# Performance work log

Hardware: AMD Instinct MI355X
Metric: run time of the kernel (lower is better)

Reference implementation:

```python
import jax, jax.numpy as jnp
import numpy as np

D_INPUT, D_MODEL, D_STATE, D_DISCR, KER = 1024, 2048, 16, 128, 4

def setup_inputs() -> dict:
    key = jax.random.key(0)
    ks = jax.random.split(key, 10)
    sc = lambda fan_in: 1.0 / np.sqrt(fan_in)
    seq = jax.random.normal(ks[0], (2, 1024, D_INPUT), dtype=jnp.float32)
    W_in = jax.random.uniform(ks[1], (2 * D_MODEL, D_INPUT), jnp.float32, -sc(D_INPUT), sc(D_INPUT))
    W_out = jax.random.uniform(ks[2], (D_INPUT, D_MODEL), jnp.float32, -sc(D_MODEL), sc(D_MODEL))
    W_sB = jax.random.uniform(ks[3], (D_STATE, D_MODEL), jnp.float32, -sc(D_MODEL), sc(D_MODEL))
    W_sC = jax.random.uniform(ks[4], (D_STATE, D_MODEL), jnp.float32, -sc(D_MODEL), sc(D_MODEL))
    W_sD1 = jax.random.uniform(ks[5], (D_DISCR, D_MODEL), jnp.float32, -sc(D_MODEL), sc(D_MODEL))
    W_sD2 = jax.random.uniform(ks[6], (D_MODEL, D_DISCR), jnp.float32, -sc(D_DISCR), sc(D_DISCR))
    conv_w = jax.random.uniform(ks[7], (D_MODEL, 1, KER), jnp.float32, -sc(KER), sc(KER))
    conv_b = jax.random.uniform(ks[8], (D_MODEL,), jnp.float32, -sc(KER), sc(KER))
    A_param = jnp.tile(jnp.arange(1, D_STATE + 1, dtype=jnp.float32), (D_MODEL, 1))
    D_param = jnp.ones((D_MODEL,), dtype=jnp.float32)
    return dict(seq=seq, W_in=W_in, W_out=W_out, W_sB=W_sB, W_sC=W_sC,
                W_sD1=W_sD1, W_sD2=W_sD2, conv_w=conv_w, conv_b=conv_b,
                A_param=A_param, D_param=D_param)

def _mamba_fwd(seq, W_in, W_out, W_sB, W_sC, W_sD1, W_sD2, conv_w, conv_b, A_param, D_param):
    b, l, _ = seq.shape
    ab = seq @ W_in.T                                   # [b,l,2*dm]
    a, g = jnp.split(ab, 2, axis=-1)
    # causal depthwise conv: torch pads ker-1 both sides then trims [..., :l]
    x = jnp.swapaxes(a, 1, 2)                           # [b,dm,l]
    y = jax.lax.conv_general_dilated(
        x, conv_w, window_strides=(1,), padding=[(KER - 1, 0)],
        dimension_numbers=('NCH', 'OIH', 'NCH'), feature_group_count=D_MODEL)
    y = y + conv_b[None, :, None]
    a = jax.nn.silu(jnp.swapaxes(y, 1, 2))              # [b,l,dm]
    # SSM
    B = a @ W_sB.T                                      # [b,l,s]
    C = a @ W_sC.T                                      # [b,l,s]
    s_delta = jax.nn.softplus(D_param + (a @ W_sD1.T) @ W_sD2.T)  # [b,l,dm]
    expA = jnp.exp(-A_param)                            # [dm,s]
    A_bar = expA[None, None] * s_delta[..., None]       # [b,l,dm,s]
    X_bar = B[:, :, None, :] * s_delta[..., None] * a[..., None]  # [b,l,dm,s]
    A_t = jnp.moveaxis(A_bar, 1, 0)                     # [l,b,dm,s]
    X_t = jnp.moveaxis(X_bar, 1, 0)
    h0 = jnp.zeros((b, D_MODEL, D_STATE), dtype=seq.dtype)
    def step(h, ax):
        At, Xt = ax
        h = At * h + Xt
        return h, h
    _, hid = jax.lax.scan(step, h0, (A_t, X_t))         # hid: [l,b,dm,s]
    out_ssm = jnp.einsum('lbds,lbs->lbd', hid, jnp.moveaxis(C, 1, 0))
    out_ssm = jnp.moveaxis(out_ssm, 0, 1) + D_param * a # [b,l,dm]
    out = (out_ssm * jax.nn.silu(g)) @ W_out.T          # [b,l,d_input]
    return out

def reference(seq, W_in, W_out, W_sB, W_sC, W_sD1, W_sD2, conv_w, conv_b, A_param, D_param):
    return _mamba_fwd(seq, W_in, W_out, W_sB, W_sC, W_sD1, W_sD2, conv_w, conv_b, A_param, D_param)
```

## Files before the change

kernel.cpp:

```cpp
#include <hip/hip_runtime.h>
#include <math.h>

#define DI 1024
#define DM 2048
#define DS 16
#define LSEQ 1024
#define NB 2
#define NTOK (NB * LSEQ)
#define TC 128
#define WU 32
#define LDU 164
#define NRP 161
#define ZLD 68
#define NZ 8

typedef unsigned short ushort_t;
typedef __attribute__((ext_vector_type(8))) short short8;
typedef __attribute__((ext_vector_type(4))) float f32x4;

__device__ __forceinline__ float bf2f(ushort_t u) {
    union { unsigned u; float f; } c; c.u = (unsigned)u << 16; return c.f;
}
__device__ __forceinline__ ushort_t f2bf(float f) {
    union { float f; unsigned u; } c; c.f = f;
    unsigned r = c.u + 0x7FFFu + ((c.u >> 16) & 1u);
    return (ushort_t)(r >> 16);
}

__device__ __forceinline__ void gload16(const void* g, void* l) {
    __builtin_amdgcn_global_load_lds(
        (const __attribute__((address_space(1))) void*)g,
        (__attribute__((address_space(3))) void*)l, 16, 0, 0);
}

template<int CTRL>
__device__ __forceinline__ float dpp_mv(float v) {
    int r = __builtin_amdgcn_update_dpp(0, __builtin_bit_cast(int, v), CTRL, 0xF, 0xF, true);
    return __builtin_bit_cast(float, r);
}
__device__ __forceinline__ float sum4(float v) {
    v += dpp_mv<0xB1>(v);
    v += dpp_mv<0x4E>(v);
    return v;
}

__device__ __forceinline__ void cvt4(const float* __restrict__ in,
                                     ushort_t* __restrict__ out, int q) {
    float4 v = ((const float4*)in)[q];
    ushort4 o;
    o.x = f2bf(v.x); o.y = f2bf(v.y); o.z = f2bf(v.z); o.w = f2bf(v.w);
    ((ushort4*)out)[q] = o;
}

__global__ __launch_bounds__(256) void prep(
    const float* __restrict__ seq, const float* __restrict__ W_in,
    const float* __restrict__ W_out, const float* __restrict__ W_sD2,
    const float* __restrict__ Wb, const float* __restrict__ Wc,
    const float* __restrict__ Wd1,
    ushort_t* __restrict__ seq_bf, ushort_t* __restrict__ W_in_bf,
    ushort_t* __restrict__ W_out_bf, ushort_t* __restrict__ W_sD2_bf,
    ushort_t* __restrict__ wbcd)
{
    int q = blockIdx.x * 256 + threadIdx.x;
    if (q < 524288)        cvt4(seq,   seq_bf,   q);
    else if (q < 1572864)  cvt4(W_in,  W_in_bf,  q - 524288);
    else if (q < 2097152)  cvt4(W_out, W_out_bf, q - 1572864);
    else if (q < 2162688)  cvt4(W_sD2, W_sD2_bf, q - 2097152);
    else {
        int p = q - 2162688;
        int idx = p * 4;
        int row = idx >> 11, col = idx & (DM - 1);
        float4 v = make_float4(0.f, 0.f, 0.f, 0.f);
        if (row < 16)       v = *(const float4*)&Wb[row * DM + col];
        else if (row < 32)  v = *(const float4*)&Wc[(row - 16) * DM + col];
        else if (row < 160) v = *(const float4*)&Wd1[(row - 32) * DM + col];
        ushort4 o;
        o.x = f2bf(v.x); o.y = f2bf(v.y); o.z = f2bf(v.z); o.w = f2bf(v.w);
        ((ushort4*)wbcd)[p] = o;
    }
}

template<int TM, int EPI, bool ASUM8 = false>
__global__ __launch_bounds__(256) void gemm_bt(
    const ushort_t* __restrict__ A, const ushort_t* __restrict__ B,
    void* __restrict__ Cout, int K, int lda, int ldb, int ldc,
    const float* __restrict__ bias, void* __restrict__ Cpart, size_t pstride)
{
    constexpr int MF = TM / 32;
    constexpr int ASZ = TM * 32;
    constexpr int BSZ = 128 * 32;
    __shared__ ushort_t As[2 * ASZ];
    __shared__ ushort_t Bs[2 * BSZ];
    const int tid = threadIdx.x;
    const int lane = tid & 63;
    const int wv = tid >> 6;
    const int wr = wv >> 1, wc = wv & 1;

    const int gx = gridDim.x, gy = gridDim.y;
    const int nwg = gx * gy;
    const int orig = blockIdx.y * gx + blockIdx.x;
    const int q8 = nwg >> 3, r8 = nwg & 7;
    const int xcd = orig & 7, i8 = orig >> 3;
    const int wg = ((xcd < r8) ? xcd * (q8 + 1) : r8 * (q8 + 1) + (xcd - r8) * q8) + i8;
    const int bm = (wg / gx) * TM, bn = (wg % gx) * 128;

    int kbeg = 0, kend = K;
    if (EPI == 5) { int ks = K / gridDim.z; kbeg = blockIdx.z * ks; kend = kbeg + ks; }

    f32x4 acc[MF][4];
#pragma unroll
    for (int m = 0; m < MF; ++m)
#pragma unroll
        for (int n = 0; n < 4; ++n) acc[m][n] = (f32x4){0.f, 0.f, 0.f, 0.f};

    const int r_lo = lane >> 2;
    const int s_l = lane & 3;
    const int row0 = wv * 16 + r_lo;
    const int row1 = 64 + wv * 16 + r_lo;
    const int sg0 = s_l ^ ((row0 >> 1) & 3);
    const int sg1 = s_l ^ ((row1 >> 1) & 3);
    const ushort_t* gB0 = B + (size_t)(bn + row0) * ldb + sg0 * 8;
    const ushort_t* gB1 = B + (size_t)(bn + row1) * ldb + sg1 * 8;
    const int lB0o = (wv * 16) * 32;
    const int lB1o = (64 + wv * 16) * 32;

    if constexpr (ASUM8) {
        const int r = tid >> 2, s = tid & 3;
        const int sg = s ^ ((r >> 1) & 3);
        const ushort_t* gA = A + (size_t)(bm + r) * lda + sg * 8;
        for (int k = kbeg; k < kend; k += 32) {
            gload16(gB0 + k, &Bs[lB0o]);
            gload16(gB1 + k, &Bs[lB1o]);
            float fa[8];
#pragma unroll
            for (int j = 0; j < 8; ++j) fa[j] = 0.f;
#pragma unroll
            for (int zz = 0; zz < NZ; ++zz) {
                const ushort_t* p = gA + (size_t)zz * pstride + k;
                ushort4 v0 = *(const ushort4*)p;
                ushort4 v1 = *(const ushort4*)(p + 4);
                fa[0] += bf2f(v0.x); fa[1] += bf2f(v0.y);
                fa[2] += bf2f(v0.z); fa[3] += bf2f(v0.w);
                fa[4] += bf2f(v1.x); fa[5] += bf2f(v1.y);
                fa[6] += bf2f(v1.z); fa[7] += bf2f(v1.w);
            }
            ushort4 o0, o1;
            o0.x = f2bf(fa[0]); o0.y = f2bf(fa[1]); o0.z = f2bf(fa[2]); o0.w = f2bf(fa[3]);
            o1.x = f2bf(fa[4]); o1.y = f2bf(fa[5]); o1.z = f2bf(fa[6]); o1.w = f2bf(fa[7]);
            *(ushort4*)&As[r * 32 + s * 8] = o0;
            *(ushort4*)&As[r * 32 + s * 8 + 4] = o1;
            __syncthreads();
            short8 af[MF], bfr[4];
#pragma unroll
            for (int m = 0; m < MF; ++m) {
                int row = wr * (TM / 2) + m * 16 + (lane & 15);
                int sl = (lane >> 4) ^ ((row >> 1) & 3);
                af[m] = *(const short8*)&As[row * 32 + sl * 8];
            }
#pragma unroll
            for (int n = 0; n < 4; ++n) {
                int row = wc * 64 + n * 16 + (lane & 15);
                int sl = (lane >> 4) ^ ((row >> 1) & 3);
                bfr[n] = *(const short8*)&Bs[row * 32 + sl * 8];
            }
#pragma unroll
            for (int m = 0; m < MF; ++m)
#pragma unroll
                for (int n = 0; n < 4; ++n)
                    acc[m][n] = __builtin_amdgcn_mfma_f32_16x16x32_bf16(af[m], bfr[n], acc[m][n], 0, 0, 0);
            __syncthreads();
        }
    } else {
        const ushort_t* gA0 = A + (size_t)(bm + row0) * lda + sg0 * 8;
        const ushort_t* gA1 = A + (size_t)(bm + row1) * lda + sg1 * 8;
        const int lA0o = (wv * 16) * 32;
        const int lA1o = ((TM == 128 ? 64 : 0) + wv * 16) * 32;

        gload16(gA0 + kbeg, &As[lA0o]);
        if (TM == 128) gload16(gA1 + kbeg, &As[lA1o]);
        gload16(gB0 + kbeg, &Bs[lB0o]);
        gload16(gB1 + kbeg, &Bs[lB1o]);
        __syncthreads();

        int cur = 0;
        for (int k = kbeg; k < kend; k += 32) {
            const int nxt = cur ^ 1;
            if (k + 32 < kend) {
                gload16(gA0 + k + 32, &As[nxt * ASZ + lA0o]);
                if (TM == 128) gload16(gA1 + k + 32, &As[nxt * ASZ + lA1o]);
                gload16(gB0 + k + 32, &Bs[nxt * BSZ + lB0o]);
                gload16(gB1 + k + 32, &Bs[nxt * BSZ + lB1o]);
            }
            const int ca = cur * ASZ, cb = cur * BSZ;
            short8 af[MF], bfr[4];
#pragma unroll
            for (int m = 0; m < MF; ++m) {
                int row = wr * (TM / 2) + m * 16 + (lane & 15);
                int sl = (lane >> 4) ^ ((row >> 1) & 3);
                af[m] = *(const short8*)&As[ca + row * 32 + sl * 8];
            }
#pragma unroll
            for (int n = 0; n < 4; ++n) {
                int row = wc * 64 + n * 16 + (lane & 15);
                int sl = (lane >> 4) ^ ((row >> 1) & 3);
                bfr[n] = *(const short8*)&Bs[cb + row * 32 + sl * 8];
            }
#pragma unroll
            for (int m = 0; m < MF; ++m)
#pragma unroll
                for (int n = 0; n < 4; ++n)
                    acc[m][n] = __builtin_amdgcn_mfma_f32_16x16x32_bf16(af[m], bfr[n], acc[m][n], 0, 0, 0);
            __syncthreads();
            cur = nxt;
        }
    }

    const int orow = bm + wr * (TM / 2) + ((lane >> 4) << 2);
    const int ocol = bn + wc * 64 + (lane & 15);
#pragma unroll
    for (int m = 0; m < MF; ++m)
#pragma unroll
        for (int n = 0; n < 4; ++n) {
            int col = ocol + n * 16;
#pragma unroll
            for (int r = 0; r < 4; ++r) {
                int row = orow + m * 16 + r;
                float v = acc[m][n][r];
                if (EPI == 3) {
                    v += bias[col];
                    v = (v > 20.f) ? v : __logf(1.f + __expf(v));
                    ((ushort_t*)Cout)[(size_t)row * ldc + col] = f2bf(v);
                } else if (EPI == 1) {
                    ((ushort_t*)Cout)[(size_t)row * ldc + col] = f2bf(v);
                } else if (EPI == 5) {
                    ((ushort_t*)Cpart + (size_t)blockIdx.z * pstride)[(size_t)row * ldc + col] = f2bf(v);
                } else {
                    ((float*)Cout)[(size_t)row * ldc + col] = v;
                }
            }
        }
}

__global__ __launch_bounds__(256) void reduce_out(const ushort_t* __restrict__ part,
                                                  float* __restrict__ out)
{
    int q = blockIdx.x * 256 + threadIdx.x;
    float sx = 0.f, sy = 0.f, sz = 0.f, sw = 0.f;
#pragma unroll
    for (int z = 0; z < 4; ++z) {
        ushort4 v = ((const ushort4*)part)[q + z * 524288];
        sx += bf2f(v.x); sy += bf2f(v.y); sz += bf2f(v.z); sw += bf2f(v.w);
    }
    float4 o; o.x = sx; o.y = sy; o.z = sz; o.w = sw;
    ((float4*)out)[q] = o;
}

__global__ __launch_bounds__(256) void conv_silu(const ushort_t* __restrict__ ab,
                                                 const float* __restrict__ w,
                                                 const float* __restrict__ bias,
                                                 ushort_t* __restrict__ outh) {
    const int bt = blockIdx.x;
    const int b = bt >> 10, t = bt & (LSEQ - 1);
    const int d = threadIdx.x * 8;

    float wv[8][4];
#pragma unroll
    for (int j = 0; j < 8; ++j) {
        float4 tw = *(const float4*)&w[(d + j) * 4];
        wv[j][0] = tw.x; wv[j][1] = tw.y; wv[j][2] = tw.z; wv[j][3] = tw.w;
    }
    float accv[8];
    {
        float4 b0 = *(const float4*)&bias[d];
        float4 b1 = *(const float4*)&bias[d + 4];
        accv[0] = b0.x; accv[1] = b0.y; accv[2] = b0.z; accv[3] = b0.w;
        accv[4] = b1.x; accv[5] = b1.y; accv[6] = b1.z; accv[7] = b1.w;
    }
#pragma unroll
    for (int k = 0; k < 4; ++k) {
        int tt = t + k - 3;
        if (tt >= 0) {
            short8 av = *(const short8*)&ab[(size_t)(b * LSEQ + tt) * (2 * DM) + d];
#pragma unroll
            for (int j = 0; j < 8; ++j)
                accv[j] = fmaf(bf2f((ushort_t)av[j]), wv[j][k], accv[j]);
        }
    }
    short8 o;
#pragma unroll
    for (int j = 0; j < 8; ++j) {
        float s = accv[j] / (1.f + __expf(-accv[j]));
        o[j] = (short)f2bf(s);
    }
    *(short8*)&outh[(size_t)bt * DM + d] = o;
}

__global__ __launch_bounds__(256) void scan_win(
    const ushort_t* __restrict__ sdel, const ushort_t* __restrict__ aconv,
    const ushort_t* __restrict__ partK, const ushort_t* __restrict__ ab,
    const float* __restrict__ A_param, const float* __restrict__ D_param,
    ushort_t* __restrict__ z)
{
    __shared__ ushort_t Ssh[64 * LDU];
    __shared__ ushort_t Vsh[64 * LDU];
    __shared__ float    Bq[4 * NRP * 4];
    __shared__ float    Cq[4 * NRP * 4];
    __shared__ ushort_t Zsh[TC * ZLD];

    const int tid = threadIdx.x;
    const int d0 = blockIdx.x * 64;
    const int c = blockIdx.y, b = blockIdx.z;
    const int nw = (c == 0) ? 0 : WU;
    const int nrows = nw + TC;
    const int tok0 = b * LSEQ + c * TC - nw;
    const int tokout0 = b * LSEQ + c * TC;

    for (int j = tid; j < (nrows / 4) * 32; j += 256) {
        int a = j & 1;
        int r = j >> 1;
        int cq = (r & 15) * 4;
        int row4 = (r >> 4) * 4;
        const ushort_t* src = (a ? aconv : sdel) + (size_t)(tok0 + row4) * DM + d0 + cq;
        ushort4 v0 = *(const ushort4*)(src);
        ushort4 v1 = *(const ushort4*)(src + DM);
        ushort4 v2 = *(const ushort4*)(src + 2 * DM);
        ushort4 v3 = *(const ushort4*)(src + 3 * DM);
        ushort_t* dst = (a ? Vsh : Ssh) + row4;
        *(ushort4*)(dst + (cq + 0) * LDU) = make_ushort4(v0.x, v1.x, v2.x, v3.x);
        *(ushort4*)(dst + (cq + 1) * LDU) = make_ushort4(v0.y, v1.y, v2.y, v3.y);
        *(ushort4*)(dst + (cq + 2) * LDU) = make_ushort4(v0.z, v1.z, v2.z, v3.z);
        *(ushort4*)(dst + (cq + 3) * LDU) = make_ushort4(v0.w, v1.w, v2.w, v3.w);
    }
    for (int j = tid; j < nrows * 8; j += 256) {
        int row = j >> 3, p = j & 7, g = p & 3;
        size_t off = (size_t)(tok0 + row) * 256 + ((p < 4) ? 4 * g : 16 + 4 * g);
        float fx = 0.f, fy = 0.f, fz = 0.f, fw = 0.f;
#pragma unroll
        for (int zz = 0; zz < NZ; ++zz) {
            ushort4 v = *(const ushort4*)&partK[(size_t)zz * (2048 * 256) + off];
            fx += bf2f(v.x); fy += bf2f(v.y); fz += bf2f(v.z); fw += bf2f(v.w);
        }
        float* dst = ((p < 4) ? Bq : Cq) + (g * NRP + row) * 4;
        *(float4*)dst = make_float4(fx, fy, fz, fw);
    }
    __syncthreads();

    const int q = tid & 3, dl = tid >> 2;
    const int d = d0 + dl;
    float4 av4 = *(const float4*)&A_param[d * DS + 4 * q];
    const float ea0 = __expf(-av4.x), ea1 = __expf(-av4.y);
    const float ea2 = __expf(-av4.z), ea3 = __expf(-av4.w);
    const float Dp = D_param[d];
    float h0 = 0.f, h1 = 0.f, h2 = 0.f, h3 = 0.f;

#define SCAN_STEP_WU(SD, AV, BI) {                                    \
        float sd = (SD), x = sd * (AV);                               \
        float4 Bv = *(const float4*)&Bq[(q * NRP + (BI)) * 4];        \
        h0 = fmaf(sd * ea0, h0, x * Bv.x);                           \
        h1 = fmaf(sd * ea1, h1, x * Bv.y);                           \
        h2 = fmaf(sd * ea2, h2, x * Bv.z);                           \
        h3 = fmaf(sd * ea3, h3, x * Bv.w); }

    for (int i4 = 0; i4 < nw; i4 += 4) {
        ushort4 sdv = *(const ushort4*)&Ssh[dl * LDU + i4];
        ushort4 avv = *(const ushort4*)&Vsh[dl * LDU + i4];
        SCAN_STEP_WU(bf2f(sdv.x), bf2f(avv.x), i4 + 0);
        SCAN_STEP_WU(bf2f(sdv.y), bf2f(avv.y), i4 + 1);
        SCAN_STEP_WU(bf2f(sdv.z), bf2f(avv.z), i4 + 2);
        SCAN_STEP_WU(bf2f(sdv.w), bf2f(avv.w), i4 + 3);
    }

#define SCAN_STEP_OUT(SD, AV, BI, RV) {                               \
        float sd = (SD), av_ = (AV), x = sd * av_;                    \
        float4 Bv = *(const float4*)&Bq[(q * NRP + (BI)) * 4];        \
        float4 Cv = *(const float4*)&Cq[(q * NRP + (BI)) * 4];        \
        h0 = fmaf(sd * ea0, h0, x * Bv.x);                           \
        h1 = fmaf(sd * ea1, h1, x * Bv.y);                           \
        h2 = fmaf(sd * ea2, h2, x * Bv.z);                           \
        h3 = fmaf(sd * ea3, h3, x * Bv.w);                           \
        float r = h0 * Cv.x;                                          \
        r = fmaf(h1, Cv.y, r); r = fmaf(h2, Cv.z, r);                 \
        r = fmaf(h3, Cv.w, r);                                        \
        r = sum4(r);                                                  \
        RV = fmaf(Dp, av_, r); }

    for (int i4 = nw; i4 < nrows; i4 += 4) {
        ushort4 sdv = *(const ushort4*)&Ssh[dl * LDU + i4];
        ushort4 avv = *(const ushort4*)&Vsh[dl * LDU + i4];
        float rv0, rv1, rv2, rv3;
        SCAN_STEP_OUT(bf2f(sdv.x), bf2f(avv.x), i4 + 0, rv0);
        SCAN_STEP_OUT(bf2f(sdv.y), bf2f(avv.y), i4 + 1, rv1);
        SCAN_STEP_OUT(bf2f(sdv.z), bf2f(avv.z), i4 + 2, rv2);
        SCAN_STEP_OUT(bf2f(sdv.w), bf2f(avv.w), i4 + 3, rv3);
        float rvq = (q == 0) ? rv0 : (q == 1) ? rv1 : (q == 2) ? rv2 : rv3;
        int io = i4 - nw;
        Zsh[(io + q) * ZLD + dl] = f2bf(rvq);
    }
    __syncthreads();
    for (int j = tid; j < TC * 16; j += 256) {
        int row = j >> 4, cq = (j & 15) * 4;
        ushort4 ov = *(const ushort4*)&Zsh[row * ZLD + cq];
        ushort4 gv = *(const ushort4*)&ab[(size_t)(tokout0 + row) * (2 * DM) + DM + d0 + cq];
        ushort4 o;
        float g0 = bf2f(gv.x), g1 = bf2f(gv.y), g2 = bf2f(gv.z), g3 = bf2f(gv.w);
        o.x = f2bf(bf2f(ov.x) * (g0 / (1.f + __expf(-g0))));
        o.y = f2bf(bf2f(ov.y) * (g1 / (1.f + __expf(-g1))));
        o.z = f2bf(bf2f(ov.z) * (g2 / (1.f + __expf(-g2))));
        o.w = f2bf(bf2f(ov.w) * (g3 / (1.f + __expf(-g3))));
        *(ushort4*)&z[(size_t)(tokout0 + row) * DM + d0 + cq] = o;
    }
#undef SCAN_STEP_WU
#undef SCAN_STEP_OUT
}

extern "C" void kernel_launch(void* const* d_in, const int* in_sizes, int n_in,
                              void* d_out, int out_size, void* d_ws, size_t ws_size,
                              hipStream_t stream) {
    const float* seq    = (const float*)d_in[0];
    const float* W_in   = (const float*)d_in[1];
    const float* W_out  = (const float*)d_in[2];
    const float* W_sB   = (const float*)d_in[3];
    const float* W_sC   = (const float*)d_in[4];
    const float* W_sD1  = (const float*)d_in[5];
    const float* W_sD2  = (const float*)d_in[6];
    const float* conv_w = (const float*)d_in[7];
    const float* conv_b = (const float*)d_in[8];
    const float* A_par  = (const float*)d_in[9];
    const float* D_par  = (const float*)d_in[10];
    float* out = (float*)d_out;

    char* ws = (char*)d_ws;
    const size_t MiB = 1024 * 1024;
    ushort_t* ab_bf    = (ushort_t*)(ws);
    ushort_t* part_out = (ushort_t*)(ws);
    ushort_t* aconv_h  = (ushort_t*)(ws + 16 * MiB);
    ushort_t* sdel_h   = (ushort_t*)(ws + 24 * MiB);
    ushort_t* W_out_bf = (ushort_t*)(ws + 32 * MiB);
    ushort_t* W_sD2_bf = (ushort_t*)(ws + 37 * MiB);
    ushort_t* Wbcd     = (ushort_t*)(ws + 37 * MiB + 512*1024);
    ushort_t* seq_bf   = (ushort_t*)(ws + 39 * MiB);
    ushort_t* W_in_bf  = (ushort_t*)(ws + 43 * MiB);
    ushort_t* partK    = (ushort_t*)(ws + 43 * MiB);
    ushort_t* z_bf     = (ushort_t*)(ws + 63 * MiB);

    dim3 blk(256);

    prep<<<dim3(8960), blk, 0, stream>>>(seq, W_in, W_out, W_sD2, W_sB, W_sC, W_sD1,
                                         seq_bf, W_in_bf, W_out_bf, W_sD2_bf, Wbcd);

    gemm_bt<64, 1><<<dim3(32, 32), blk, 0, stream>>>(seq_bf, W_in_bf, ab_bf, 1024, DI, DI, 2 * DM, nullptr, nullptr, 0);

    conv_silu<<<dim3(NTOK), blk, 0, stream>>>(ab_bf, conv_w, conv_b, aconv_h);

    gemm_bt<64, 5><<<dim3(2, 32, 8), blk, 0, stream>>>(aconv_h, Wbcd, nullptr, DM, DM, DM, 256, nullptr, partK, 2048 * 256);

    gemm_bt<64, 3, true><<<dim3(16, 32), blk, 0, stream>>>(partK + 32, W_sD2_bf, sdel_h, 128, 256, 128, DM, D_par, nullptr, 2048 * 256);

    scan_win<<<dim3(DM / 64, LSEQ / TC, NB), blk, 0, stream>>>(
        sdel_h, aconv_h, partK, ab_bf, A_par, D_par, z_bf);

    gemm_bt<64, 5><<<dim3(8, 32, 4), blk, 0, stream>>>(z_bf, W_out_bf, nullptr, DM, DM, DM, DI, nullptr, part_out, 2048 * 1024);

    reduce_out<<<dim3(2048), blk, 0, stream>>>(part_out, out);
}
```

Before: 128.2 us.

## Overlap late weight conversions with input GEMM via extra block row

```diff
diff --git a/kernel.cpp b/kernel.cpp
--- a/kernel.cpp
+++ b/kernel.cpp
@@ -54,38 +54,44 @@
 
 __global__ __launch_bounds__(256) void prep(
     const float* __restrict__ seq, const float* __restrict__ W_in,
-    const float* __restrict__ W_out, const float* __restrict__ W_sD2,
-    const float* __restrict__ Wb, const float* __restrict__ Wc,
-    const float* __restrict__ Wd1,
-    ushort_t* __restrict__ seq_bf, ushort_t* __restrict__ W_in_bf,
-    ushort_t* __restrict__ W_out_bf, ushort_t* __restrict__ W_sD2_bf,
-    ushort_t* __restrict__ wbcd)
+    ushort_t* __restrict__ seq_bf, ushort_t* __restrict__ W_in_bf)
 {
     int q = blockIdx.x * 256 + threadIdx.x;
-    if (q < 524288)        cvt4(seq,   seq_bf,   q);
-    else if (q < 1572864)  cvt4(W_in,  W_in_bf,  q - 524288);
-    else if (q < 2097152)  cvt4(W_out, W_out_bf, q - 1572864);
-    else if (q < 2162688)  cvt4(W_sD2, W_sD2_bf, q - 2097152);
-    else {
-        int p = q - 2162688;
-        int idx = p * 4;
-        int row = idx >> 11, col = idx & (DM - 1);
-        float4 v = make_float4(0.f, 0.f, 0.f, 0.f);
-        if (row < 16)       v = *(const float4*)&Wb[row * DM + col];
-        else if (row < 32)  v = *(const float4*)&Wc[(row - 16) * DM + col];
-        else if (row < 160) v = *(const float4*)&Wd1[(row - 32) * DM + col];
-        ushort4 o;
-        o.x = f2bf(v.x); o.y = f2bf(v.y); o.z = f2bf(v.z); o.w = f2bf(v.w);
-        ((ushort4*)wbcd)[p] = o;
-    }
-}
-
-template<int TM, int EPI, bool ASUM8 = false>
+    if (q < 524288) cvt4(seq, seq_bf, q);
+    else            cvt4(W_in, W_in_bf, q - 524288);
+}
+
+template<int TM, int EPI, bool ASUM8 = false, bool CVT = false>
 __global__ __launch_bounds__(256) void gemm_bt(
     const ushort_t* __restrict__ A, const ushort_t* __restrict__ B,
     void* __restrict__ Cout, int K, int lda, int ldb, int ldc,
-    const float* __restrict__ bias, void* __restrict__ Cpart, size_t pstride)
+    const float* __restrict__ bias, void* __restrict__ Cpart, size_t pstride,
+    const float* __restrict__ cW_out = nullptr, const float* __restrict__ cW_sD2 = nullptr,
+    const float* __restrict__ cWb = nullptr, const float* __restrict__ cWc = nullptr,
+    const float* __restrict__ cWd1 = nullptr,
+    ushort_t* __restrict__ dW_out = nullptr, ushort_t* __restrict__ dW_sD2 = nullptr,
+    ushort_t* __restrict__ dwbcd = nullptr)
 {
+    if (CVT && (int)blockIdx.y == (int)gridDim.y - 1) {
+        for (int q = blockIdx.x * 256 + threadIdx.x; q < 720896; q += 32 * 256) {
+            if (q < 524288)      cvt4(cW_out, dW_out, q);
+            else if (q < 589824) cvt4(cW_sD2, dW_sD2, q - 524288);
+            else {
+                int p = q - 589824;
+                int idx = p * 4;
+                int row = idx >> 11, col = idx & (DM - 1);
+                float4 v = make_float4(0.f, 0.f, 0.f, 0.f);
+                if (row < 16)       v = *(const float4*)&cWb[row * DM + col];
+                else if (row < 32)  v = *(const float4*)&cWc[(row - 16) * DM + col];
+                else if (row < 160) v = *(const float4*)&cWd1[(row - 32) * DM + col];
+                ushort4 o;
+                o.x = f2bf(v.x); o.y = f2bf(v.y); o.z = f2bf(v.z); o.w = f2bf(v.w);
+                ((ushort4*)dwbcd)[p] = o;
+            }
+        }
+        return;
+    }
+
     constexpr int MF = TM / 32;
     constexpr int ASZ = TM * 32;
     constexpr int BSZ = 128 * 32;
@@ -96,7 +102,7 @@
     const int wv = tid >> 6;
     const int wr = wv >> 1, wc = wv & 1;
 
-    const int gx = gridDim.x, gy = gridDim.y;
+    const int gx = gridDim.x, gy = (int)gridDim.y - (CVT ? 1 : 0);
     const int nwg = gx * gy;
     const int orig = blockIdx.y * gx + blockIdx.x;
     const int q8 = nwg >> 3, r8 = nwg & 7;
@@ -331,17 +337,27 @@
         *(ushort4*)(dst + (cq + 2) * LDU) = make_ushort4(v0.z, v1.z, v2.z, v3.z);
         *(ushort4*)(dst + (cq + 3) * LDU) = make_ushort4(v0.w, v1.w, v2.w, v3.w);
     }
-    for (int j = tid; j < nrows * 8; j += 256) {
-        int row = j >> 3, p = j & 7, g = p & 3;
-        size_t off = (size_t)(tok0 + row) * 256 + ((p < 4) ? 4 * g : 16 + 4 * g);
+    for (int j = tid; j < nrows * 4; j += 256) {
+        int row = j >> 2, g = j & 3;
+        size_t off = (size_t)(tok0 + row) * 256 + 4 * g;
         float fx = 0.f, fy = 0.f, fz = 0.f, fw = 0.f;
 #pragma unroll
         for (int zz = 0; zz < NZ; ++zz) {
             ushort4 v = *(const ushort4*)&partK[(size_t)zz * (2048 * 256) + off];
             fx += bf2f(v.x); fy += bf2f(v.y); fz += bf2f(v.z); fw += bf2f(v.w);
         }
-        float* dst = ((p < 4) ? Bq : Cq) + (g * NRP + row) * 4;
-        *(float4*)dst = make_float4(fx, fy, fz, fw);
+        *(float4*)&Bq[(g * NRP + row) * 4] = make_float4(fx, fy, fz, fw);
+    }
+    for (int j = tid; j < TC * 4; j += 256) {
+        int row = nw + (j >> 2), g = j & 3;
+        size_t off = (size_t)(tok0 + row) * 256 + 16 + 4 * g;
+        float fx = 0.f, fy = 0.f, fz = 0.f, fw = 0.f;
+#pragma unroll
+        for (int zz = 0; zz < NZ; ++zz) {
+            ushort4 v = *(const ushort4*)&partK[(size_t)zz * (2048 * 256) + off];
+            fx += bf2f(v.x); fy += bf2f(v.y); fz += bf2f(v.z); fw += bf2f(v.w);
+        }
+        *(float4*)&Cq[(g * NRP + row) * 4] = make_float4(fx, fy, fz, fw);
     }
     __syncthreads();
 
@@ -445,10 +461,11 @@
 
     dim3 blk(256);
 
-    prep<<<dim3(8960), blk, 0, stream>>>(seq, W_in, W_out, W_sD2, W_sB, W_sC, W_sD1,
-                                         seq_bf, W_in_bf, W_out_bf, W_sD2_bf, Wbcd);
-
-    gemm_bt<64, 1><<<dim3(32, 32), blk, 0, stream>>>(seq_bf, W_in_bf, ab_bf, 1024, DI, DI, 2 * DM, nullptr, nullptr, 0);
+    prep<<<dim3(6144), blk, 0, stream>>>(seq, W_in, seq_bf, W_in_bf);
+
+    gemm_bt<64, 1, false, true><<<dim3(32, 33), blk, 0, stream>>>(
+        seq_bf, W_in_bf, ab_bf, 1024, DI, DI, 2 * DM, nullptr, nullptr, 0,
+        W_out, W_sD2, W_sB, W_sC, W_sD1, W_out_bf, W_sD2_bf, Wbcd);
 
     conv_silu<<<dim3(NTOK), blk, 0, stream>>>(ab_bf, conv_w, conv_b, aconv_h);
 
```

New measurement: 152.0 us. +18.5%, slower.

## Replace split-K bf16 partial buffers with fp32 atomic accumulation

Applied to the files above, without the earlier changes.

```diff
diff --git a/kernel.cpp b/kernel.cpp
--- a/kernel.cpp
+++ b/kernel.cpp
@@ -12,7 +12,6 @@
 #define LDU 164
 #define NRP 161
 #define ZLD 68
-#define NZ 8
 
 typedef unsigned short ushort_t;
 typedef __attribute__((ext_vector_type(8))) short short8;
@@ -80,11 +79,11 @@
     }
 }
 
-template<int TM, int EPI, bool ASUM8 = false>
+template<int TM, int EPI, bool AF32 = false>
 __global__ __launch_bounds__(256) void gemm_bt(
     const ushort_t* __restrict__ A, const ushort_t* __restrict__ B,
     void* __restrict__ Cout, int K, int lda, int ldb, int ldc,
-    const float* __restrict__ bias, void* __restrict__ Cpart, size_t pstride)
+    const float* __restrict__ bias)
 {
     constexpr int MF = TM / 32;
     constexpr int ASZ = TM * 32;
@@ -105,7 +104,7 @@
     const int bm = (wg / gx) * TM, bn = (wg % gx) * 128;
 
     int kbeg = 0, kend = K;
-    if (EPI == 5) { int ks = K / gridDim.z; kbeg = blockIdx.z * ks; kend = kbeg + ks; }
+    if (gridDim.z > 1) { int ks = K / gridDim.z; kbeg = blockIdx.z * ks; kend = kbeg + ks; }
 
     f32x4 acc[MF][4];
 #pragma unroll
@@ -124,29 +123,18 @@
     const int lB0o = (wv * 16) * 32;
     const int lB1o = (64 + wv * 16) * 32;
 
-    if constexpr (ASUM8) {
+    if constexpr (AF32) {
         const int r = tid >> 2, s = tid & 3;
         const int sg = s ^ ((r >> 1) & 3);
-        const ushort_t* gA = A + (size_t)(bm + r) * lda + sg * 8;
+        const float* pA = reinterpret_cast<const float*>(A) + (size_t)(bm + r) * lda + sg * 8;
         for (int k = kbeg; k < kend; k += 32) {
             gload16(gB0 + k, &Bs[lB0o]);
             gload16(gB1 + k, &Bs[lB1o]);
-            float fa[8];
-#pragma unroll
-            for (int j = 0; j < 8; ++j) fa[j] = 0.f;
-#pragma unroll
-            for (int zz = 0; zz < NZ; ++zz) {
-                const ushort_t* p = gA + (size_t)zz * pstride + k;
-                ushort4 v0 = *(const ushort4*)p;
-                ushort4 v1 = *(const ushort4*)(p + 4);
-                fa[0] += bf2f(v0.x); fa[1] += bf2f(v0.y);
-                fa[2] += bf2f(v0.z); fa[3] += bf2f(v0.w);
-                fa[4] += bf2f(v1.x); fa[5] += bf2f(v1.y);
-                fa[6] += bf2f(v1.z); fa[7] += bf2f(v1.w);
-            }
+            float4 v0 = *(const float4*)(pA + k);
+            float4 v1 = *(const float4*)(pA + k + 4);
             ushort4 o0, o1;
-            o0.x = f2bf(fa[0]); o0.y = f2bf(fa[1]); o0.z = f2bf(fa[2]); o0.w = f2bf(fa[3]);
-            o1.x = f2bf(fa[4]); o1.y = f2bf(fa[5]); o1.z = f2bf(fa[6]); o1.w = f2bf(fa[7]);
+            o0.x = f2bf(v0.x); o0.y = f2bf(v0.y); o0.z = f2bf(v0.z); o0.w = f2bf(v0.w);
+            o1.x = f2bf(v1.x); o1.y = f2bf(v1.y); o1.z = f2bf(v1.z); o1.w = f2bf(v1.w);
             *(ushort4*)&As[r * 32 + s * 8] = o0;
             *(ushort4*)&As[r * 32 + s * 8 + 4] = o1;
             __syncthreads();
@@ -232,8 +220,8 @@
                     ((ushort_t*)Cout)[(size_t)row * ldc + col] = f2bf(v);
                 } else if (EPI == 1) {
                     ((ushort_t*)Cout)[(size_t)row * ldc + col] = f2bf(v);
-                } else if (EPI == 5) {
-                    ((ushort_t*)Cpart + (size_t)blockIdx.z * pstride)[(size_t)row * ldc + col] = f2bf(v);
+                } else if (EPI == 6) {
+                    atomicAdd(&((float*)Cout)[(size_t)row * ldc + col], v);
                 } else {
                     ((float*)Cout)[(size_t)row * ldc + col] = v;
                 }
@@ -241,27 +229,16 @@
         }
 }
 
-__global__ __launch_bounds__(256) void reduce_out(const ushort_t* __restrict__ part,
-                                                  float* __restrict__ out)
-{
-    int q = blockIdx.x * 256 + threadIdx.x;
-    float sx = 0.f, sy = 0.f, sz = 0.f, sw = 0.f;
-#pragma unroll
-    for (int z = 0; z < 4; ++z) {
-        ushort4 v = ((const ushort4*)part)[q + z * 524288];
-        sx += bf2f(v.x); sy += bf2f(v.y); sz += bf2f(v.z); sw += bf2f(v.w);
-    }
-    float4 o; o.x = sx; o.y = sy; o.z = sz; o.w = sw;
-    ((float4*)out)[q] = o;
-}
-
 __global__ __launch_bounds__(256) void conv_silu(const ushort_t* __restrict__ ab,
                                                  const float* __restrict__ w,
                                                  const float* __restrict__ bias,
-                                                 ushort_t* __restrict__ outh) {
+                                                 ushort_t* __restrict__ outh,
+                                                 float* __restrict__ bcd1f) {
     const int bt = blockIdx.x;
     const int b = bt >> 10, t = bt & (LSEQ - 1);
     const int d = threadIdx.x * 8;
+
+    bcd1f[(size_t)bt * 256 + threadIdx.x] = 0.f;
 
     float wv[8][4];
 #pragma unroll
@@ -297,9 +274,9 @@
 
 __global__ __launch_bounds__(256) void scan_win(
     const ushort_t* __restrict__ sdel, const ushort_t* __restrict__ aconv,
-    const ushort_t* __restrict__ partK, const ushort_t* __restrict__ ab,
+    const float* __restrict__ bcd1f, const ushort_t* __restrict__ ab,
     const float* __restrict__ A_param, const float* __restrict__ D_param,
-    ushort_t* __restrict__ z)
+    ushort_t* __restrict__ z, float* __restrict__ outZero)
 {
     __shared__ ushort_t Ssh[64 * LDU];
     __shared__ ushort_t Vsh[64 * LDU];
@@ -314,6 +291,14 @@
     const int nrows = nw + TC;
     const int tok0 = b * LSEQ + c * TC - nw;
     const int tokout0 = b * LSEQ + c * TC;
+
+    {
+        const int bid = blockIdx.x + (blockIdx.y << 5) + (blockIdx.z << 8);
+        float4 z4 = make_float4(0.f, 0.f, 0.f, 0.f);
+#pragma unroll
+        for (int j = 0; j < 4; ++j)
+            ((float4*)outZero)[(size_t)bid * 1024 + j * 256 + tid] = z4;
+    }
 
     for (int j = tid; j < (nrows / 4) * 32; j += 256) {
         int a = j & 1;
@@ -331,17 +316,15 @@
         *(ushort4*)(dst + (cq + 2) * LDU) = make_ushort4(v0.z, v1.z, v2.z, v3.z);
         *(ushort4*)(dst + (cq + 3) * LDU) = make_ushort4(v0.w, v1.w, v2.w, v3.w);
     }
-    for (int j = tid; j < nrows * 8; j += 256) {
-        int row = j >> 3, p = j & 7, g = p & 3;
-        size_t off = (size_t)(tok0 + row) * 256 + ((p < 4) ? 4 * g : 16 + 4 * g);
-        float fx = 0.f, fy = 0.f, fz = 0.f, fw = 0.f;
-#pragma unroll
-        for (int zz = 0; zz < NZ; ++zz) {
-            ushort4 v = *(const ushort4*)&partK[(size_t)zz * (2048 * 256) + off];
-            fx += bf2f(v.x); fy += bf2f(v.y); fz += bf2f(v.z); fw += bf2f(v.w);
-        }
-        float* dst = ((p < 4) ? Bq : Cq) + (g * NRP + row) * 4;
-        *(float4*)dst = make_float4(fx, fy, fz, fw);
+    for (int j = tid; j < nrows * 4; j += 256) {
+        int row = j >> 2, g = j & 3;
+        float4 f = *(const float4*)&bcd1f[(size_t)(tok0 + row) * 256 + 4 * g];
+        *(float4*)&Bq[(g * NRP + row) * 4] = f;
+    }
+    for (int j = tid; j < TC * 4; j += 256) {
+        int row = nw + (j >> 2), g = j & 3;
+        float4 f = *(const float4*)&bcd1f[(size_t)(tok0 + row) * 256 + 16 + 4 * g];
+        *(float4*)&Cq[(g * NRP + row) * 4] = f;
     }
     __syncthreads();
 
@@ -432,7 +415,6 @@
     char* ws = (char*)d_ws;
     const size_t MiB = 1024 * 1024;
     ushort_t* ab_bf    = (ushort_t*)(ws);
-    ushort_t* part_out = (ushort_t*)(ws);
     ushort_t* aconv_h  = (ushort_t*)(ws + 16 * MiB);
     ushort_t* sdel_h   = (ushort_t*)(ws + 24 * MiB);
     ushort_t* W_out_bf = (ushort_t*)(ws + 32 * MiB);
@@ -440,7 +422,7 @@
     ushort_t* Wbcd     = (ushort_t*)(ws + 37 * MiB + 512*1024);
     ushort_t* seq_bf   = (ushort_t*)(ws + 39 * MiB);
     ushort_t* W_in_bf  = (ushort_t*)(ws + 43 * MiB);
-    ushort_t* partK    = (ushort_t*)(ws + 43 * MiB);
+    float*    bcd1f    = (float*)(ws + 43 * MiB);
     ushort_t* z_bf     = (ushort_t*)(ws + 63 * MiB);
 
     dim3 blk(256);
@@ -448,18 +430,17 @@
     prep<<<dim3(8960), blk, 0, stream>>>(seq, W_in, W_out, W_sD2, W_sB, W_sC, W_sD1,
                                          seq_bf, W_in_bf, W_out_bf, W_sD2_bf, Wbcd);
 
-    gemm_bt<64, 1><<<dim3(32, 32), blk, 0, stream>>>(seq_bf, W_in_bf, ab_bf, 1024, DI, DI, 2 * DM, nullptr, nullptr, 0);
-
-    conv_silu<<<dim3(NTOK), blk, 0, stream>>>(ab_bf, conv_w, conv_b, aconv_h);
-
-    gemm_bt<64, 5><<<dim3(2, 32, 8), blk, 0, stream>>>(aconv_h, Wbcd, nullptr, DM, DM, DM, 256, nullptr, partK, 2048 * 256);
-
-    gemm_bt<64, 3, true><<<dim3(16, 32), blk, 0, stream>>>(partK + 32, W_sD2_bf, sdel_h, 128, 256, 128, DM, D_par, nullptr, 2048 * 256);
+    gemm_bt<64, 1><<<dim3(32, 32), blk, 0, stream>>>(seq_bf, W_in_bf, ab_bf, 1024, DI, DI, 2 * DM, nullptr);
+
+    conv_silu<<<dim3(NTOK), blk, 0, stream>>>(ab_bf, conv_w, conv_b, aconv_h, bcd1f);
+
+    gemm_bt<64, 6><<<dim3(2, 32, 8), blk, 0, stream>>>(aconv_h, Wbcd, bcd1f, DM, DM, DM, 256, nullptr);
+
+    gemm_bt<64, 3, true><<<dim3(16, 32), blk, 0, stream>>>(
+        (const ushort_t*)(bcd1f + 32), W_sD2_bf, sdel_h, 128, 256, 128, DM, D_par);
 
     scan_win<<<dim3(DM / 64, LSEQ / TC, NB), blk, 0, stream>>>(
-        sdel_h, aconv_h, partK, ab_bf, A_par, D_par, z_bf);
-
-    gemm_bt<64, 5><<<dim3(8, 32, 4), blk, 0, stream>>>(z_bf, W_out_bf, nullptr, DM, DM, DM, DI, nullptr, part_out, 2048 * 1024);
-
-    reduce_out<<<dim3(2048), blk, 0, stream>>>(part_out, out);
-}
+        sdel_h, aconv_h, bcd1f, ab_bf, A_par, D_par, z_bf, out);
+
+    gemm_bt<64, 6><<<dim3(8, 32, 4), blk, 0, stream>>>(z_bf, W_out_bf, out, DM, DM, DM, DI, nullptr);
+}
```

New measurement: 149.6 us. +16.7%, slower.
